# Kernel optimization log

Measured on AMD Instinct MI355X. Metric: run time of the kernel, lower is better.

## Reference

```python
import jax, jax.numpy as jnp
import numpy as np

EMBED_DIM = 768
Q_DIM = 64
V_DIM = 64
WINDOW_SIZE = 3


def setup_inputs() -> dict:
    key = jax.random.key(0)
    ks = jax.random.split(key, 7)
    B, N = 4, 4096
    s = 1.0 / np.sqrt(EMBED_DIM)
    x = jax.random.normal(ks[0], (B, N, EMBED_DIM), dtype=jnp.float32)
    Wq = jax.random.normal(ks[1], (EMBED_DIM, Q_DIM), dtype=jnp.float32) * s
    bq = jax.random.normal(ks[2], (Q_DIM,), dtype=jnp.float32) * 0.01
    Wk = jax.random.normal(ks[3], (EMBED_DIM, Q_DIM), dtype=jnp.float32) * s
    bk = jax.random.normal(ks[4], (Q_DIM,), dtype=jnp.float32) * 0.01
    Wv = jax.random.normal(ks[5], (EMBED_DIM, V_DIM), dtype=jnp.float32) * s
    bv = jax.random.normal(ks[6], (V_DIM,), dtype=jnp.float32) * 0.01
    return {"x": x, "Wq": Wq, "bq": bq, "Wk": Wk, "bk": bk, "Wv": Wv, "bv": bv}


def reference(x, Wq, bq, Wk, bk, Wv, bv):
    # Faithful translation of SliddingWindowAttention.forward, including the
    # original's quirk: diagonal scores are written into columns 0..window_size-1
    # of a full (B, N, N) zero matrix, softmax is taken over ALL N columns
    # (zeros included), and the result is matmul'd with V.
    B, N, _ = x.shape
    Q = x @ Wq + bq  # (B, N, Q_DIM)
    K = x @ Wk + bk  # (B, N, Q_DIM)
    V = x @ Wv + bv  # (B, N, V_DIM)

    half = WINDOW_SIZE // 2
    columns = jnp.zeros((B, N, N), dtype=x.dtype)
    for idx, di in enumerate(range(-half, half + 1)):
        # diagonal offset di: pair row i with column j = i + di (valid rows only)
        rows = np.arange(max(0, -di), N - max(0, di))
        cols_j = rows + di
        c = jnp.einsum('bid,bid->bi', Q[:, rows, :], K[:, cols_j, :])
        columns = columns.at[:, rows, idx].set(c)

    attn = jax.nn.softmax(columns, axis=2)  # (B, N, N)
    return attn @ V  # (B, N, V_DIM)
```

## Files before the change

kernel.cpp:

```cpp
#include <hip/hip_runtime.h>
#include <hip/hip_bf16.h>
#include <math.h>

#define EMBED 768
#define NTOK  4096
#define NB    4
#define ROWS  16384
#define CN    192

typedef __attribute__((ext_vector_type(8))) short bf16x8;
typedef __attribute__((ext_vector_type(8))) unsigned short u16x8;
typedef __attribute__((ext_vector_type(4))) float f32x4;

__device__ inline void split2(float f, short& h, short& l) {
  union { float f; unsigned u; } a; a.f = f;
  unsigned r = (a.u + 0x7FFFu + ((a.u >> 16) & 1u)) & 0xFFFF0000u;
  h = (short)(r >> 16);
  union { unsigned u; float f; } hf; hf.u = r;
  union { float f; unsigned u; } b; b.f = f - hf.f;
  l = (short)((b.u + 0x7FFFu + ((b.u >> 16) & 1u)) >> 16);
}

__global__ __launch_bounds__(256) void wprep(const float* __restrict__ Wq,
                                             const float* __restrict__ Wk,
                                             const float* __restrict__ Wv,
                                             unsigned short* __restrict__ Wt,
                                             float* __restrict__ Vsum) {
  __shared__ float tile[32 * 64];
  const int b   = blockIdx.x;
  const int mat = b / 24;
  const int ks  = b - mat * 24;
  const float* W = (mat == 0) ? Wq : (mat == 1) ? Wk : Wv;
  const int t = threadIdx.x;

  const float4* src = (const float4*)(W + ks * 2048);
  ((float4*)tile)[t]       = src[t];
  ((float4*)tile)[t + 256] = src[t + 256];
  __syncthreads();

  const int q    = t >> 6;
  const int nloc = t & 63;
  u16x8 hv, lv;
#pragma unroll
  for (int j = 0; j < 8; ++j) {
    short h, l;
    split2(tile[(q * 8 + j) * 64 + nloc], h, l);
    hv[j] = (unsigned short)h;
    lv[j] = (unsigned short)l;
  }
  const size_t base = (size_t)ks * 12288 + (size_t)q * 1536 + (size_t)(mat * 64 + nloc) * 8;
  *(u16x8*)(Wt + base)        = hv;
  *(u16x8*)(Wt + base + 6144) = lv;

  if (b == 0 && t < NB * 64) Vsum[t] = 0.f;
}

__device__ inline void gload_lds16(const unsigned short* g, unsigned short* l) {
  __builtin_amdgcn_global_load_lds(
      (const __attribute__((address_space(1))) unsigned int*)(g),
      (__attribute__((address_space(3))) unsigned int*)(l),
      16, 0, 0);
}

#define STAGE(LB, KS) do {                                            \
    const unsigned short* _g = Wtu + (size_t)(KS) * 12288 + tid * 8;  \
    unsigned short* _l = (LB) + tid * 8;                              \
    gload_lds16(_g,          _l);                                     \
    gload_lds16(_g + 2048,   _l + 2048);                              \
    gload_lds16(_g + 4096,   _l + 4096);                              \
    gload_lds16(_g + 6144,   _l + 6144);                              \
    gload_lds16(_g + 8192,   _l + 8192);                              \
    gload_lds16(_g + 10240,  _l + 10240);                             \
  } while (0)

__device__ inline void splitHW(float f, short& h, short& l) {
  __hip_bfloat16 hb = __float2bfloat16(f);
  float hf = __bfloat162float(hb);
  __hip_bfloat16 lb = __float2bfloat16(f - hf);
  h = __builtin_bit_cast(short, hb);
  l = __builtin_bit_cast(short, lb);
}

__device__ inline void cvt8hw(const float4 f0, const float4 f1, bf16x8& h, bf16x8& l) {
  short hh, ll;
  splitHW(f0.x, hh, ll); h[0] = hh; l[0] = ll;
  splitHW(f0.y, hh, ll); h[1] = hh; l[1] = ll;
  splitHW(f0.z, hh, ll); h[2] = hh; l[2] = ll;
  splitHW(f0.w, hh, ll); h[3] = hh; l[3] = ll;
  splitHW(f1.x, hh, ll); h[4] = hh; l[4] = ll;
  splitHW(f1.y, hh, ll); h[5] = hh; l[5] = ll;
  splitHW(f1.z, hh, ll); h[6] = hh; l[6] = ll;
  splitHW(f1.w, hh, ll); h[7] = hh; l[7] = ll;
}

#define DO_NT3(LBP, NT, ACC0, ACC1) do {                                       \
    bf16x8 _bh = *(const bf16x8*)((LBP) + (NT) * 128);                         \
    bf16x8 _bl = *(const bf16x8*)((LBP) + (NT) * 128 + 6144);                  \
    ACC0 = __builtin_amdgcn_mfma_f32_16x16x32_bf16(ah0, _bh, ACC0, 0, 0, 0);   \
    ACC0 = __builtin_amdgcn_mfma_f32_16x16x32_bf16(ah0, _bl, ACC0, 0, 0, 0);   \
    ACC0 = __builtin_amdgcn_mfma_f32_16x16x32_bf16(al0, _bh, ACC0, 0, 0, 0);   \
    ACC1 = __builtin_amdgcn_mfma_f32_16x16x32_bf16(ah1, _bh, ACC1, 0, 0, 0);   \
    ACC1 = __builtin_amdgcn_mfma_f32_16x16x32_bf16(ah1, _bl, ACC1, 0, 0, 0);   \
    ACC1 = __builtin_amdgcn_mfma_f32_16x16x32_bf16(al1, _bh, ACC1, 0, 0, 0);   \
  } while (0)

#define COMPUTE(LB, A00, A01, A10, A11) do {                          \
    bf16x8 ah0, al0, ah1, al1;                                        \
    cvt8hw(A00, A01, ah0, al0);                                       \
    cvt8hw(A10, A11, ah1, al1);                                       \
    const unsigned short* _lb = (LB) + lbo;                           \
    DO_NT3(_lb, 0, acc00, acc10);                                     \
    DO_NT3(_lb, 1, acc01, acc11);                                     \
    DO_NT3(_lb, 2, acc02, acc12);                                     \
  } while (0)

__global__ __launch_bounds__(256, 2) void qkv_mfma(const float* __restrict__ x,
                                                   const unsigned short* __restrict__ Wtu,
                                                   const float* __restrict__ bq,
                                                   const float* __restrict__ bk,
                                                   const float* __restrict__ bv,
                                                   float* __restrict__ C,
                                                   float* __restrict__ Vsum) {
  __shared__ unsigned short lbuf0[12288];
  __shared__ unsigned short lbuf1[12288];

  const int tid  = threadIdx.x;
  const int lane = tid & 63;
  const int wn   = tid >> 6;
  const int ml   = lane & 15;
  const int q    = lane >> 4;
  const int r0   = blockIdx.x * 32;
  const int lbo  = q * 1536 + (wn * 48 + ml) * 8;

  f32x4 acc00 = {0.f,0.f,0.f,0.f}, acc01 = {0.f,0.f,0.f,0.f}, acc02 = {0.f,0.f,0.f,0.f};
  f32x4 acc10 = {0.f,0.f,0.f,0.f}, acc11 = {0.f,0.f,0.f,0.f}, acc12 = {0.f,0.f,0.f,0.f};

  const float* xa0 = x + (size_t)(r0 + ml) * EMBED + q * 8;
  const float* xa1 = xa0 + (size_t)16 * EMBED;

  STAGE(lbuf0, 0);
  float4 a00 = *(const float4*)xa0;
  float4 a01 = *(const float4*)(xa0 + 4);
  float4 a10 = *(const float4*)xa1;
  float4 a11 = *(const float4*)(xa1 + 4);

  for (int ks = 0; ks < 24; ks += 2) {
    __syncthreads();
    STAGE(lbuf1, ks + 1);
    float4 n00 = *(const float4*)(xa0 + 32);
    float4 n01 = *(const float4*)(xa0 + 36);
    float4 n10 = *(const float4*)(xa1 + 32);
    float4 n11 = *(const float4*)(xa1 + 36);
    COMPUTE(lbuf0, a00, a01, a10, a11);

    __syncthreads();
    if (ks < 22) {
      STAGE(lbuf0, ks + 2);
      a00 = *(const float4*)(xa0 + 64);
      a01 = *(const float4*)(xa0 + 68);
      a10 = *(const float4*)(xa1 + 64);
      a11 = *(const float4*)(xa1 + 68);
    }
    COMPUTE(lbuf1, n00, n01, n10, n11);
    xa0 += 64; xa1 += 64;
  }

#define EPI(NT, ACC, MF) do {                                               \
    const int n = wn * 48 + (NT) * 16 + ml;                                 \
    const float bias = (n < 64) ? bq[n] : (n < 128) ? bk[n - 64] : bv[n - 128]; \
    const int row = r0 + (MF) * 16 + q * 4;                                 \
    C[(size_t)(row + 0) * CN + n] = ACC[0] + bias;                          \
    C[(size_t)(row + 1) * CN + n] = ACC[1] + bias;                          \
    C[(size_t)(row + 2) * CN + n] = ACC[2] + bias;                          \
    C[(size_t)(row + 3) * CN + n] = ACC[3] + bias;                          \
  } while (0)

  EPI(0, acc00, 0); EPI(1, acc01, 0); EPI(2, acc02, 0);
  EPI(0, acc10, 1); EPI(1, acc11, 1); EPI(2, acc12, 1);

#define VS(NT, ACC0, ACC1) do {                                             \
    const int n = wn * 48 + (NT) * 16 + ml;                                 \
    if (n >= 128) {                                                         \
      float s = ACC0[0] + ACC0[1] + ACC0[2] + ACC0[3]                       \
              + ACC1[0] + ACC1[1] + ACC1[2] + ACC1[3] + 8.f * bv[n - 128];  \
      s += __shfl_xor(s, 16, 64);                                           \
      s += __shfl_xor(s, 32, 64);                                           \
      if (q == 0) atomicAdd(&Vsum[(r0 >> 12) * 64 + (n - 128)], s);         \
    }                                                                       \
  } while (0)

  VS(0, acc00, acc10); VS(1, acc01, acc11); VS(2, acc02, acc12);
}

__global__ __launch_bounds__(256) void attn_kernel(const float* __restrict__ C,
                                                   const float* __restrict__ Vsum,
                                                   float* __restrict__ out) {
  const int t    = threadIdx.x;
  const int lane = t & 63;
  const int wave = t >> 6;
  const int r = blockIdx.x * 4 + wave;
  const int b = r >> 12;
  const int i = r & (NTOK - 1);

  const float q  = C[(size_t)r * CN + lane];
  const float kc = C[(size_t)r * CN + 64 + lane];
  float km = 0.f, kp = 0.f;
  if (i > 0)        km = C[(size_t)(r - 1) * CN + 64 + lane];
  if (i < NTOK - 1) kp = C[(size_t)(r + 1) * CN + 64 + lane];

  float p0 = q * km, p1 = q * kc, p2 = q * kp;
#pragma unroll
  for (int off = 32; off > 0; off >>= 1) {
    p0 += __shfl_xor(p0, off, 64);
    p1 += __shfl_xor(p1, off, 64);
    p2 += __shfl_xor(p2, off, 64);
  }

  const float s0 = (i > 0) ? p0 : 0.f;
  const float s1 = p1;
  const float s2 = (i < NTOK - 1) ? p2 : 0.f;
  const float m  = fmaxf(fmaxf(s0, s1), fmaxf(s2, 0.f));
  const float e0 = expf(s0 - m);
  const float e1 = expf(s1 - m);
  const float e2 = expf(s2 - m);
  const float ez = expf(-m);
  const float Z  = e0 + e1 + e2 + (float)(NTOK - 3) * ez;

  const size_t vb = ((size_t)b * NTOK) * CN + 128;
  const float v0 = C[vb + lane];
  const float v1 = C[vb + CN + lane];
  const float v2 = C[vb + 2 * (size_t)CN + lane];
  const float vs = Vsum[b * 64 + lane];

  out[(size_t)r * 64 + lane] =
      (e0 * v0 + e1 * v1 + e2 * v2 + ez * (vs - v0 - v1 - v2)) / Z;
}

extern "C" void kernel_launch(void* const* d_in, const int* in_sizes, int n_in,
                              void* d_out, int out_size, void* d_ws, size_t ws_size,
                              hipStream_t stream) {
  const float* x  = (const float*)d_in[0];
  const float* Wq = (const float*)d_in[1];
  const float* bq = (const float*)d_in[2];
  const float* Wk = (const float*)d_in[3];
  const float* bk = (const float*)d_in[4];
  const float* Wv = (const float*)d_in[5];
  const float* bv = (const float*)d_in[6];
  float* out = (float*)d_out;

  float* C    = (float*)d_ws;
  float* Vsum = C + (size_t)ROWS * CN;
  unsigned short* Wt = (unsigned short*)(Vsum + NB * 64);

  wprep<<<72, 256, 0, stream>>>(Wq, Wk, Wv, Wt, Vsum);
  qkv_mfma<<<512, 256, 0, stream>>>(x, Wt, bq, bk, bv, C, Vsum);
  attn_kernel<<<ROWS / 4, 256, 0, stream>>>(C, Vsum, out);
}
```

Baseline: 133.5 us.

## Drop LDS staging in QKV GEMM; load weights directly into registers with 8 waves

The weight tiles are no longer staged through LDS with global_load_lds and barriers. Each wave now reads its B fragments straight from global memory (L2) into registers with a software double-buffer. Blocks grow to 512 threads, and the 32-row tile is split across two wave halves, so each wave holds 3 accumulators instead of 6. This removes the __syncthreads and LDS traffic, but the waves in a block now fetch the same weight data from cache redundantly.

```diff
diff --git a/kernel.cpp b/kernel.cpp
--- a/kernel.cpp
+++ b/kernel.cpp
@@ -55,23 +55,6 @@
   if (b == 0 && t < NB * 64) Vsum[t] = 0.f;
 }
 
-__device__ inline void gload_lds16(const unsigned short* g, unsigned short* l) {
-  __builtin_amdgcn_global_load_lds(
-      (const __attribute__((address_space(1))) unsigned int*)(g),
-      (__attribute__((address_space(3))) unsigned int*)(l),
-      16, 0, 0);
-}
-
-#define STAGE(LB, KS) do {                                            \
-    const unsigned short* _g = Wtu + (size_t)(KS) * 12288 + tid * 8;  \
-    unsigned short* _l = (LB) + tid * 8;                              \
-    gload_lds16(_g,          _l);                                     \
-    gload_lds16(_g + 2048,   _l + 2048);                              \
-    gload_lds16(_g + 4096,   _l + 4096);                              \
-    gload_lds16(_g + 6144,   _l + 6144);                              \
-    gload_lds16(_g + 8192,   _l + 8192);                              \
-    gload_lds16(_g + 10240,  _l + 10240);                             \
-  } while (0)
 
 __device__ inline void splitHW(float f, short& h, short& l) {
   __hip_bfloat16 hb = __float2bfloat16(f);
@@ -93,103 +76,94 @@
   splitHW(f1.w, hh, ll); h[7] = hh; l[7] = ll;
 }
 
-#define DO_NT3(LBP, NT, ACC0, ACC1) do {                                       \
-    bf16x8 _bh = *(const bf16x8*)((LBP) + (NT) * 128);                         \
-    bf16x8 _bl = *(const bf16x8*)((LBP) + (NT) * 128 + 6144);                  \
-    ACC0 = __builtin_amdgcn_mfma_f32_16x16x32_bf16(ah0, _bh, ACC0, 0, 0, 0);   \
-    ACC0 = __builtin_amdgcn_mfma_f32_16x16x32_bf16(ah0, _bl, ACC0, 0, 0, 0);   \
-    ACC0 = __builtin_amdgcn_mfma_f32_16x16x32_bf16(al0, _bh, ACC0, 0, 0, 0);   \
-    ACC1 = __builtin_amdgcn_mfma_f32_16x16x32_bf16(ah1, _bh, ACC1, 0, 0, 0);   \
-    ACC1 = __builtin_amdgcn_mfma_f32_16x16x32_bf16(ah1, _bl, ACC1, 0, 0, 0);   \
-    ACC1 = __builtin_amdgcn_mfma_f32_16x16x32_bf16(al1, _bh, ACC1, 0, 0, 0);   \
-  } while (0)
-
-#define COMPUTE(LB, A00, A01, A10, A11) do {                          \
-    bf16x8 ah0, al0, ah1, al1;                                        \
-    cvt8hw(A00, A01, ah0, al0);                                       \
-    cvt8hw(A10, A11, ah1, al1);                                       \
-    const unsigned short* _lb = (LB) + lbo;                           \
-    DO_NT3(_lb, 0, acc00, acc10);                                     \
-    DO_NT3(_lb, 1, acc01, acc11);                                     \
-    DO_NT3(_lb, 2, acc02, acc12);                                     \
-  } while (0)
-
-__global__ __launch_bounds__(256, 2) void qkv_mfma(const float* __restrict__ x,
+#define LOADB(H0, L0, H1, L1, H2, L2, KS) do {                        \
+    const bf16x8* _p = (const bf16x8*)(Bb + (size_t)(KS) * 12288);    \
+    H0 = _p[0];  L0 = _p[768];                                        \
+    H1 = _p[16]; L1 = _p[784];                                        \
+    H2 = _p[32]; L2 = _p[800];                                        \
+  } while (0)
+
+#define LOADA(A0, A1, KS) do {                                        \
+    A0 = *(const float4*)(xa + (KS) * 32);                            \
+    A1 = *(const float4*)(xa + (KS) * 32 + 4);                        \
+  } while (0)
+
+#define COMPUTE(A0, A1, H0, L0, H1, L1, H2, L2) do {                              \
+    bf16x8 ah, al;                                                                \
+    cvt8hw(A0, A1, ah, al);                                                       \
+    acc0 = __builtin_amdgcn_mfma_f32_16x16x32_bf16(ah, H0, acc0, 0, 0, 0);        \
+    acc1 = __builtin_amdgcn_mfma_f32_16x16x32_bf16(ah, H1, acc1, 0, 0, 0);        \
+    acc2 = __builtin_amdgcn_mfma_f32_16x16x32_bf16(ah, H2, acc2, 0, 0, 0);        \
+    acc0 = __builtin_amdgcn_mfma_f32_16x16x32_bf16(ah, L0, acc0, 0, 0, 0);        \
+    acc1 = __builtin_amdgcn_mfma_f32_16x16x32_bf16(ah, L1, acc1, 0, 0, 0);        \
+    acc2 = __builtin_amdgcn_mfma_f32_16x16x32_bf16(ah, L2, acc2, 0, 0, 0);        \
+    acc0 = __builtin_amdgcn_mfma_f32_16x16x32_bf16(al, H0, acc0, 0, 0, 0);        \
+    acc1 = __builtin_amdgcn_mfma_f32_16x16x32_bf16(al, H1, acc1, 0, 0, 0);        \
+    acc2 = __builtin_amdgcn_mfma_f32_16x16x32_bf16(al, H2, acc2, 0, 0, 0);        \
+  } while (0)
+
+__global__ __launch_bounds__(512, 4) void qkv_mfma(const float* __restrict__ x,
                                                    const unsigned short* __restrict__ Wtu,
                                                    const float* __restrict__ bq,
                                                    const float* __restrict__ bk,
                                                    const float* __restrict__ bv,
                                                    float* __restrict__ C,
                                                    float* __restrict__ Vsum) {
-  __shared__ unsigned short lbuf0[12288];
-  __shared__ unsigned short lbuf1[12288];
-
   const int tid  = threadIdx.x;
   const int lane = tid & 63;
-  const int wn   = tid >> 6;
+  const int wv   = tid >> 6;
+  const int mh   = wv & 1;
+  const int wn   = wv >> 1;
   const int ml   = lane & 15;
   const int q    = lane >> 4;
   const int r0   = blockIdx.x * 32;
-  const int lbo  = q * 1536 + (wn * 48 + ml) * 8;
-
-  f32x4 acc00 = {0.f,0.f,0.f,0.f}, acc01 = {0.f,0.f,0.f,0.f}, acc02 = {0.f,0.f,0.f,0.f};
-  f32x4 acc10 = {0.f,0.f,0.f,0.f}, acc11 = {0.f,0.f,0.f,0.f}, acc12 = {0.f,0.f,0.f,0.f};
-
-  const float* xa0 = x + (size_t)(r0 + ml) * EMBED + q * 8;
-  const float* xa1 = xa0 + (size_t)16 * EMBED;
-
-  STAGE(lbuf0, 0);
-  float4 a00 = *(const float4*)xa0;
-  float4 a01 = *(const float4*)(xa0 + 4);
-  float4 a10 = *(const float4*)xa1;
-  float4 a11 = *(const float4*)(xa1 + 4);
+
+  f32x4 acc0 = {0.f,0.f,0.f,0.f}, acc1 = {0.f,0.f,0.f,0.f}, acc2 = {0.f,0.f,0.f,0.f};
+
+  const float* xa = x + (size_t)(r0 + mh * 16 + ml) * EMBED + q * 8;
+  const unsigned short* Bb = Wtu + q * 1536 + (wn * 48 + ml) * 8;
+
+  bf16x8 h0, l0, h1, l1, h2, l2;
+  bf16x8 g0, m0, g1, m1, g2, m2;
+  float4 a0, a1, b0, b1;
+
+  LOADB(h0, l0, h1, l1, h2, l2, 0);
+  LOADA(a0, a1, 0);
 
   for (int ks = 0; ks < 24; ks += 2) {
-    __syncthreads();
-    STAGE(lbuf1, ks + 1);
-    float4 n00 = *(const float4*)(xa0 + 32);
-    float4 n01 = *(const float4*)(xa0 + 36);
-    float4 n10 = *(const float4*)(xa1 + 32);
-    float4 n11 = *(const float4*)(xa1 + 36);
-    COMPUTE(lbuf0, a00, a01, a10, a11);
-
-    __syncthreads();
+    LOADB(g0, m0, g1, m1, g2, m2, ks + 1);
+    LOADA(b0, b1, ks + 1);
+    COMPUTE(a0, a1, h0, l0, h1, l1, h2, l2);
     if (ks < 22) {
-      STAGE(lbuf0, ks + 2);
-      a00 = *(const float4*)(xa0 + 64);
-      a01 = *(const float4*)(xa0 + 68);
-      a10 = *(const float4*)(xa1 + 64);
-      a11 = *(const float4*)(xa1 + 68);
+      LOADB(h0, l0, h1, l1, h2, l2, ks + 2);
+      LOADA(a0, a1, ks + 2);
     }
-    COMPUTE(lbuf1, n00, n01, n10, n11);
-    xa0 += 64; xa1 += 64;
+    COMPUTE(b0, b1, g0, m0, g1, m1, g2, m2);
   }
 
-#define EPI(NT, ACC, MF) do {                                               \
+#define EPI(NT, ACC) do {                                                   \
     const int n = wn * 48 + (NT) * 16 + ml;                                 \
     const float bias = (n < 64) ? bq[n] : (n < 128) ? bk[n - 64] : bv[n - 128]; \
-    const int row = r0 + (MF) * 16 + q * 4;                                 \
+    const int row = r0 + mh * 16 + q * 4;                                   \
     C[(size_t)(row + 0) * CN + n] = ACC[0] + bias;                          \
     C[(size_t)(row + 1) * CN + n] = ACC[1] + bias;                          \
     C[(size_t)(row + 2) * CN + n] = ACC[2] + bias;                          \
     C[(size_t)(row + 3) * CN + n] = ACC[3] + bias;                          \
   } while (0)
 
-  EPI(0, acc00, 0); EPI(1, acc01, 0); EPI(2, acc02, 0);
-  EPI(0, acc10, 1); EPI(1, acc11, 1); EPI(2, acc12, 1);
-
-#define VS(NT, ACC0, ACC1) do {                                             \
+  EPI(0, acc0); EPI(1, acc1); EPI(2, acc2);
+
+#define VS(NT, ACC) do {                                                    \
     const int n = wn * 48 + (NT) * 16 + ml;                                 \
     if (n >= 128) {                                                         \
-      float s = ACC0[0] + ACC0[1] + ACC0[2] + ACC0[3]                       \
-              + ACC1[0] + ACC1[1] + ACC1[2] + ACC1[3] + 8.f * bv[n - 128];  \
+      float s = ACC[0] + ACC[1] + ACC[2] + ACC[3] + 4.f * bv[n - 128];      \
       s += __shfl_xor(s, 16, 64);                                           \
       s += __shfl_xor(s, 32, 64);                                           \
       if (q == 0) atomicAdd(&Vsum[(r0 >> 12) * 64 + (n - 128)], s);         \
     }                                                                       \
   } while (0)
 
-  VS(0, acc00, acc10); VS(1, acc01, acc11); VS(2, acc02, acc12);
+  VS(0, acc0); VS(1, acc1); VS(2, acc2);
 }
 
 __global__ __launch_bounds__(256) void attn_kernel(const float* __restrict__ C,
@@ -253,6 +227,6 @@
   unsigned short* Wt = (unsigned short*)(Vsum + NB * 64);
 
   wprep<<<72, 256, 0, stream>>>(Wq, Wk, Wv, Wt, Vsum);
-  qkv_mfma<<<512, 256, 0, stream>>>(x, Wt, bq, bk, bv, C, Vsum);
+  qkv_mfma<<<512, 512, 0, stream>>>(x, Wt, bq, bk, bv, C, Vsum);
   attn_kernel<<<ROWS / 4, 256, 0, stream>>>(C, Vsum, out);
 }
```

Result: slower. 140.6 us (+5.3%).
